# Performance work log

Hardware: AMD Instinct MI355X
Metric: run time of the kernel (lower is better)

Reference implementation:

```python
import jax, jax.numpy as jnp
import numpy as np

N = 100000       # nodes
E = 1600000      # edges (avg degree 16)
IN_DIM = 64
HID_DIM = 128
OUT_DIM = 64

def setup_inputs() -> dict:
    key = jax.random.key(0)
    k = jax.random.split(key, 8)
    inp = jax.random.normal(k[0], (IN_DIM, N), dtype=jnp.float32)
    src = jax.random.randint(k[1], (E,), 0, N, dtype=jnp.int32)
    dst = jax.random.randint(k[2], (E,), 0, N, dtype=jnp.int32)
    # Linear params (torch nn.Linear: y = x @ W.T + b)
    s1 = 1.0 / np.sqrt(IN_DIM)
    W1 = jax.random.uniform(k[3], (HID_DIM, IN_DIM), jnp.float32, -s1, s1)
    b1 = jax.random.uniform(k[4], (HID_DIM,), jnp.float32, -s1, s1)
    s2 = 1.0 / np.sqrt(HID_DIM)
    W2 = jax.random.uniform(k[5], (OUT_DIM, HID_DIM), jnp.float32, -s2, s2)
    b2 = jax.random.uniform(k[6], (OUT_DIM,), jnp.float32, -s2, s2)
    return {"inp": inp, "src": src, "dst": dst, "W1": W1, "b1": b1, "W2": W2, "b2": b2}

def reference(inp, src, dst, W1, b1, W2, b2):
    # inp: [in_dim, N] (module passes transposed features)
    X = inp.T                                   # [N, in_dim] node features
    # update_all(copy_src, sum): gather src features, scatter-add at dst
    agg = jax.ops.segment_sum(X[src], dst, num_segments=X.shape[0])  # [N, in_dim]
    h = jax.nn.relu(agg @ W1.T + b1)            # [N, hidden]
    out = h @ W2.T + b2                         # [N, out_dim]
    return out.T                                 # [out_dim, N] (final .t())
```

## Files before the change

kernel.cpp:

```cpp
#include <hip/hip_runtime.h>
#include <hip/hip_bf16.h>
#include <stdint.h>

typedef unsigned short ushort_t;
using short8   = __attribute__((ext_vector_type(8))) short;
using float4v  = __attribute__((ext_vector_type(4))) float;
using uint4v   = __attribute__((ext_vector_type(4))) unsigned;

#define BSH    6
#define BUCKW  64
#define CAP    1536
#define NBMAX  2048
#define BINB   256

__device__ __forceinline__ float bf2f(ushort_t u) {
    union { unsigned int i; float f; } v;
    v.i = ((unsigned int)u) << 16;
    return v.f;
}
__device__ __forceinline__ ushort_t f2b(float f) {
    union { float f; unsigned int i; } v;
    v.f = f;
    unsigned int u = v.i;
    unsigned int r = (u + 0x7fffu + ((u >> 16) & 1u)) >> 16;
    return (ushort_t)r;
}
__device__ __forceinline__ float blo2f(unsigned v) {
    union { unsigned i; float f; } u; u.i = v << 16; return u.f;
}
__device__ __forceinline__ float bhi2f(unsigned v) {
    union { unsigned i; float f; } u; u.i = v & 0xFFFF0000u; return u.f;
}

__global__ __launch_bounds__(512) void prep_k(
        const float* __restrict__ inp, ushort_t* __restrict__ X, int N,
        const float* __restrict__ W1, const float* __restrict__ W2,
        ushort_t* __restrict__ w1b, ushort_t* __restrict__ w2b,
        const int* __restrict__ src, const int* __restrict__ dst,
        int* __restrict__ gcur, unsigned* __restrict__ bin, int E,
        int NB, int TB) {
    __shared__ int lcnt[NBMAX];
    __shared__ int gbase[NBMAX];
    __shared__ int lcur[NBMAX];
    int tid = threadIdx.x;

    if ((int)blockIdx.x < TB) {
        if (blockIdx.x == 0) {
            for (int i = tid; i < 8192; i += 512) {
                w1b[i] = f2b(W1[i]);
                w2b[i] = f2b(W2[i]);
            }
        }
        int db = tid >> 7;
        int nl = tid & 127;
        int nc = blockIdx.x * 128 + nl;
        if (nc < N) {
            const float* ip = inp + (size_t)(db * 16) * N + nc;
            float v[16];
#pragma unroll
            for (int r = 0; r < 16; ++r)
                v[r] = ip[(size_t)r * N];
            unsigned dw[8];
#pragma unroll
            for (int j = 0; j < 8; ++j)
                dw[j] = (unsigned)f2b(v[2 * j]) | ((unsigned)f2b(v[2 * j + 1]) << 16);
            unsigned* xp = (unsigned*)X + (size_t)nc * 32 + db * 8;
            uint4v a = {dw[0], dw[1], dw[2], dw[3]};
            uint4v b = {dw[4], dw[5], dw[6], dw[7]};
            *(uint4v*)(xp)     = a;
            *(uint4v*)(xp + 4) = b;
        }
    } else {
        int bid   = blockIdx.x - TB;
        int chunk = (E + BINB - 1) / BINB;
        int s0 = bid * chunk;
        int s1 = s0 + chunk;
        if (s1 > E) s1 = E;

        for (int b = tid; b < NB; b += 512) lcnt[b] = 0;
        __syncthreads();

        int e = s0 + tid;
        for (; e + 512 * 7 < s1; e += 512 * 8) {
            int d[8];
#pragma unroll
            for (int k = 0; k < 8; ++k) d[k] = dst[e + 512 * k];
#pragma unroll
            for (int k = 0; k < 8; ++k) atomicAdd(&lcnt[d[k] >> BSH], 1);
        }
        for (; e < s1; e += 512)
            atomicAdd(&lcnt[dst[e] >> BSH], 1);
        __syncthreads();

        for (int b = tid; b < NB; b += 512) {
            int c = lcnt[b];
            gbase[b] = c ? atomicAdd(&gcur[b], c) : 0;
            lcur[b]  = 0;
        }
        __syncthreads();

        e = s0 + tid;
        for (; e + 512 * 7 < s1; e += 512 * 8) {
            int d[8], s[8];
#pragma unroll
            for (int k = 0; k < 8; ++k) {
                d[k] = dst[e + 512 * k];
                s[k] = src[e + 512 * k];
            }
#pragma unroll
            for (int k = 0; k < 8; ++k) {
                int b   = d[k] >> BSH;
                int pos = gbase[b] + atomicAdd(&lcur[b], 1);
                if (pos < CAP)
                    bin[(size_t)b * CAP + pos] =
                        ((unsigned)(d[k] & (BUCKW - 1)) << 24) | (unsigned)s[k];
            }
        }
        for (; e < s1; e += 512) {
            int dv = dst[e];
            int b  = dv >> BSH;
            int pos = gbase[b] + atomicAdd(&lcur[b], 1);
            if (pos < CAP)
                bin[(size_t)b * CAP + pos] =
                    ((unsigned)(dv & (BUCKW - 1)) << 24) | (unsigned)src[e];
        }
    }
}

__global__ __launch_bounds__(256) void bagg_k(
        const unsigned* __restrict__ Xu, const unsigned* __restrict__ bin,
        const int* __restrict__ gcur, unsigned* __restrict__ aggu, int N) {
    __shared__ unsigned sl[CAP];
    __shared__ int ecnt[BUCKW];
    __shared__ int sc[BUCKW];
    __shared__ int ecur[BUCKW];
    int tid = threadIdx.x;
    int b   = blockIdx.x;
    int lo  = b << BSH;

    int cnt = gcur[b];
    if (cnt > CAP) cnt = CAP;
    const unsigned* bb = bin + (size_t)b * CAP;

    if (tid < BUCKW) ecnt[tid] = 0;
    __syncthreads();

    for (int i = tid; i < cnt; i += 256)
        atomicAdd(&ecnt[bb[i] >> 24], 1);
    __syncthreads();

    if (tid < BUCKW) sc[tid] = ecnt[tid];
    __syncthreads();
#pragma unroll
    for (int off = 1; off < BUCKW; off <<= 1) {
        int v = 0;
        if (tid < BUCKW && tid >= off) v = sc[tid - off];
        __syncthreads();
        if (tid < BUCKW) sc[tid] += v;
        __syncthreads();
    }
    if (tid < BUCKW) { sc[tid] -= ecnt[tid]; ecur[tid] = 0; }
    __syncthreads();

    for (int i = tid; i < cnt; i += 256) {
        unsigned p = bb[i];
        int nl  = (int)(p >> 24);
        int pos = sc[nl] + atomicAdd(&ecur[nl], 1);
        sl[pos] = p;
    }
    __syncthreads();

    int wave = tid >> 6;
    int lane = tid & 63;
    int half = lane >> 5;
    int c2   = lane & 31;

    for (int n = wave; n < BUCKW; n += 4) {
        int node = lo + n;
        if (node >= N) break;
        int s0 = sc[n];
        int c  = ecnt[n];
        float alo0 = 0.f, ahi0 = 0.f, alo1 = 0.f, ahi1 = 0.f;
        int i = 0;
        for (; i + 16 <= c; i += 16) {
            unsigned p0 = sl[s0 + i +  0 + half], p1 = sl[s0 + i +  2 + half];
            unsigned p2 = sl[s0 + i +  4 + half], p3 = sl[s0 + i +  6 + half];
            unsigned p4 = sl[s0 + i +  8 + half], p5 = sl[s0 + i + 10 + half];
            unsigned p6 = sl[s0 + i + 12 + half], p7 = sl[s0 + i + 14 + half];
            unsigned v0 = Xu[(size_t)(p0 & 0xFFFFFFu) * 32 + c2];
            unsigned v1 = Xu[(size_t)(p1 & 0xFFFFFFu) * 32 + c2];
            unsigned v2 = Xu[(size_t)(p2 & 0xFFFFFFu) * 32 + c2];
            unsigned v3 = Xu[(size_t)(p3 & 0xFFFFFFu) * 32 + c2];
            unsigned v4 = Xu[(size_t)(p4 & 0xFFFFFFu) * 32 + c2];
            unsigned v5 = Xu[(size_t)(p5 & 0xFFFFFFu) * 32 + c2];
            unsigned v6 = Xu[(size_t)(p6 & 0xFFFFFFu) * 32 + c2];
            unsigned v7 = Xu[(size_t)(p7 & 0xFFFFFFu) * 32 + c2];
            alo0 += blo2f(v0); ahi0 += bhi2f(v0);
            alo1 += blo2f(v1); ahi1 += bhi2f(v1);
            alo0 += blo2f(v2); ahi0 += bhi2f(v2);
            alo1 += blo2f(v3); ahi1 += bhi2f(v3);
            alo0 += blo2f(v4); ahi0 += bhi2f(v4);
            alo1 += blo2f(v5); ahi1 += bhi2f(v5);
            alo0 += blo2f(v6); ahi0 += bhi2f(v6);
            alo1 += blo2f(v7); ahi1 += bhi2f(v7);
        }
        for (; i + 2 <= c; i += 2) {
            unsigned p = sl[s0 + i + half];
            unsigned v = Xu[(size_t)(p & 0xFFFFFFu) * 32 + c2];
            alo0 += blo2f(v); ahi0 += bhi2f(v);
        }
        if (i + half < c) {
            unsigned p = sl[s0 + i + half];
            unsigned v = Xu[(size_t)(p & 0xFFFFFFu) * 32 + c2];
            alo1 += blo2f(v); ahi1 += bhi2f(v);
        }
        float alo = alo0 + alo1;
        float ahi = ahi0 + ahi1;
        float blo = __shfl(alo, lane + 32);
        float bhi = __shfl(ahi, lane + 32);
        if (half == 0) {
            alo += blo; ahi += bhi;
            aggu[(size_t)node * 32 + c2] =
                (unsigned)f2b(alo) | ((unsigned)f2b(ahi) << 16);
        }
    }
}

#define HPITCH 136

__global__ __launch_bounds__(256) void mlp_k(
        const ushort_t* __restrict__ aggb,
        const ushort_t* __restrict__ W1, const float* __restrict__ b1,
        const ushort_t* __restrict__ W2, const float* __restrict__ b2,
        float* __restrict__ out, int N) {
    __shared__ ushort_t h_s[4][16 * HPITCH];

    int wave = threadIdx.x >> 6;
    int lane = threadIdx.x & 63;
    int row  = lane & 15;
    int quad = lane >> 4;
    int n0   = blockIdx.x * 64 + wave * 16;

    int anode = n0 + row;
    if (anode > N - 1) anode = N - 1;
    const ushort_t* ap = aggb + (size_t)anode * 64;
    short8 a0 = *(const short8*)(ap + quad * 8);
    short8 a1 = *(const short8*)(ap + 32 + quad * 8);

    float4v zero = {0.f, 0.f, 0.f, 0.f};
    float4v acc[8];
#pragma unroll
    for (int nt = 0; nt < 8; ++nt) acc[nt] = zero;

#pragma unroll
    for (int nt = 0; nt < 8; ++nt) {
        const ushort_t* wp = W1 + (size_t)(nt * 16 + row) * 64 + quad * 8;
        short8 bf0 = *(const short8*)(wp);
        short8 bf1 = *(const short8*)(wp + 32);
        acc[nt] = __builtin_amdgcn_mfma_f32_16x16x32_bf16(a0, bf0, acc[nt], 0, 0, 0);
        acc[nt] = __builtin_amdgcn_mfma_f32_16x16x32_bf16(a1, bf1, acc[nt], 0, 0, 0);
    }

    ushort_t* hw = h_s[wave];
#pragma unroll
    for (int nt = 0; nt < 8; ++nt) {
        float bias = b1[nt * 16 + row];
#pragma unroll
        for (int r = 0; r < 4; ++r) {
            float v = acc[nt][r] + bias;
            v = v > 0.f ? v : 0.f;
            hw[(quad * 4 + r) * HPITCH + nt * 16 + row] = f2b(v);
        }
    }
    __syncthreads();

    short8 a2[4];
#pragma unroll
    for (int kt = 0; kt < 4; ++kt)
        a2[kt] = *(const short8*)(hw + row * HPITCH + kt * 32 + quad * 8);

    float4v acc2[4];
#pragma unroll
    for (int nt = 0; nt < 4; ++nt) acc2[nt] = zero;

#pragma unroll
    for (int nt = 0; nt < 4; ++nt) {
#pragma unroll
        for (int kt = 0; kt < 4; ++kt) {
            short8 bfr = *(const short8*)(W2 + (size_t)(nt * 16 + row) * 128 +
                                          kt * 32 + quad * 8);
            acc2[nt] = __builtin_amdgcn_mfma_f32_16x16x32_bf16(a2[kt], bfr, acc2[nt], 0, 0, 0);
        }
    }

    int node = n0 + quad * 4;
    if (node < N) {
#pragma unroll
        for (int nt = 0; nt < 4; ++nt) {
            int ko = nt * 16 + row;
            float bias = b2[ko];
            float4v pk;
#pragma unroll
            for (int r = 0; r < 4; ++r) pk[r] = acc2[nt][r] + bias;
            *(float4v*)(out + (size_t)ko * N + node) = pk;
        }
    }
}

extern "C" void kernel_launch(void* const* d_in, const int* in_sizes, int n_in,
                              void* d_out, int out_size, void* d_ws, size_t ws_size,
                              hipStream_t stream) {
    const float* inp = (const float*)d_in[0];
    const int*   src = (const int*)d_in[1];
    const int*   dst = (const int*)d_in[2];
    const float* W1  = (const float*)d_in[3];
    const float* b1  = (const float*)d_in[4];
    const float* W2  = (const float*)d_in[5];
    const float* b2  = (const float*)d_in[6];
    float* out = (float*)d_out;

    int N  = in_sizes[0] / 64;
    int E  = in_sizes[1];
    int NB = (N + BUCKW - 1) >> BSH;

    ushort_t* aggb = (ushort_t*)d_ws;
    ushort_t* w1b  = aggb + (size_t)N * 64;
    ushort_t* w2b  = w1b + 8192;
    int*      gcur = (int*)(w2b + 8192);

    char*     ob  = (char*)d_out;
    ushort_t* X   = (ushort_t*)ob;
    unsigned* bin = (unsigned*)(ob + (size_t)N * 64 * 2);

    hipMemsetAsync(gcur, 0, NB * sizeof(int), stream);

    int TB = (N + 127) / 128;
    prep_k<<<TB + BINB, 512, 0, stream>>>(inp, X, N, W1, W2, w1b, w2b,
                                          src, dst, gcur, bin, E, NB, TB);

    bagg_k<<<NB, 256, 0, stream>>>((const unsigned*)X, bin, gcur,
                                   (unsigned*)aggb, N);

    int tb = (N + 63) / 64;
    mlp_k<<<tb, 256, 0, stream>>>(aggb, w1b, b1, w2b, b2, out, N);
}
```

Measured before the change: 203.2 us.

## Fuse bucket aggregation with MLP in one kernel and widen prep blocks

Adds a fused kernel that aggregates each 64-node bucket into shared memory and runs both MFMA linear layers on it directly. This drops the global round trip of the aggregated bf16 features and one kernel launch. The shared pool is reused for the edge list and the hidden tile. The prep kernel moves to 1024-thread blocks with int4 vectorized edge loads and 32-bit index math. The fused path runs only when the workspace can hold X and the bins; otherwise the old three-kernel path is kept.

Result: slower. 212.7 us (+4.7%).

```diff
diff --git a/kernel.cpp b/kernel.cpp
--- a/kernel.cpp
+++ b/kernel.cpp
@@ -12,6 +12,8 @@
 #define CAP    1536
 #define NBMAX  2048
 #define BINB   256
+#define HPITCH 136
+#define APITCH 36
 
 __device__ __forceinline__ float bf2f(ushort_t u) {
     union { unsigned int i; float f; } v;
@@ -32,97 +34,280 @@
     union { unsigned i; float f; } u; u.i = v & 0xFFFF0000u; return u.f;
 }
 
-__global__ __launch_bounds__(512) void prep_k(
+__global__ __launch_bounds__(1024) void prep_k(
         const float* __restrict__ inp, ushort_t* __restrict__ X, int N,
         const float* __restrict__ W1, const float* __restrict__ W2,
         ushort_t* __restrict__ w1b, ushort_t* __restrict__ w2b,
         const int* __restrict__ src, const int* __restrict__ dst,
         int* __restrict__ gcur, unsigned* __restrict__ bin, int E,
-        int NB, int TB) {
+        int NB) {
     __shared__ int lcnt[NBMAX];
     __shared__ int gbase[NBMAX];
     __shared__ int lcur[NBMAX];
     int tid = threadIdx.x;
 
-    if ((int)blockIdx.x < TB) {
-        if (blockIdx.x == 0) {
-            for (int i = tid; i < 8192; i += 512) {
+    if ((int)blockIdx.x >= BINB) {
+        int tb = blockIdx.x - BINB;
+        if (tb == 0) {
+            for (int i = tid; i < 8192; i += 1024) {
                 w1b[i] = f2b(W1[i]);
                 w2b[i] = f2b(W2[i]);
             }
         }
-        int db = tid >> 7;
-        int nl = tid & 127;
-        int nc = blockIdx.x * 128 + nl;
+        int db = tid >> 8;
+        int nl = tid & 255;
+        int nc = tb * 256 + nl;
         if (nc < N) {
-            const float* ip = inp + (size_t)(db * 16) * N + nc;
+            unsigned ib = (unsigned)(db * 16) * (unsigned)N + (unsigned)nc;
             float v[16];
 #pragma unroll
             for (int r = 0; r < 16; ++r)
-                v[r] = ip[(size_t)r * N];
+                v[r] = inp[ib + (unsigned)(r * N)];
             unsigned dw[8];
 #pragma unroll
             for (int j = 0; j < 8; ++j)
                 dw[j] = (unsigned)f2b(v[2 * j]) | ((unsigned)f2b(v[2 * j + 1]) << 16);
-            unsigned* xp = (unsigned*)X + (size_t)nc * 32 + db * 8;
+            unsigned* xp = (unsigned*)X + (((unsigned)nc) << 5) + (unsigned)(db << 3);
             uint4v a = {dw[0], dw[1], dw[2], dw[3]};
             uint4v b = {dw[4], dw[5], dw[6], dw[7]};
             *(uint4v*)(xp)     = a;
             *(uint4v*)(xp + 4) = b;
         }
     } else {
-        int bid   = blockIdx.x - TB;
-        int chunk = (E + BINB - 1) / BINB;
-        int s0 = bid * chunk;
-        int s1 = s0 + chunk;
-        if (s1 > E) s1 = E;
-
-        for (int b = tid; b < NB; b += 512) lcnt[b] = 0;
-        __syncthreads();
-
-        int e = s0 + tid;
-        for (; e + 512 * 7 < s1; e += 512 * 8) {
-            int d[8];
-#pragma unroll
-            for (int k = 0; k < 8; ++k) d[k] = dst[e + 512 * k];
-#pragma unroll
-            for (int k = 0; k < 8; ++k) atomicAdd(&lcnt[d[k] >> BSH], 1);
-        }
-        for (; e < s1; e += 512)
-            atomicAdd(&lcnt[dst[e] >> BSH], 1);
-        __syncthreads();
-
-        for (int b = tid; b < NB; b += 512) {
+        int bid  = blockIdx.x;
+        int Q    = (E + 3) >> 2;
+        int chunk = (Q + BINB - 1) / BINB;
+        int q0 = bid * chunk;
+        int q1 = q0 + chunk;
+        if (q1 > Q) q1 = Q;
+        const int4* dst4 = (const int4*)dst;
+        const int4* src4 = (const int4*)src;
+
+        for (int b = tid; b < NB; b += 1024) lcnt[b] = 0;
+        __syncthreads();
+
+        for (int q = q0 + tid; q < q1; q += 1024) {
+            int e = q << 2;
+            if (e + 3 < E) {
+                int4 d = dst4[q];
+                atomicAdd(&lcnt[d.x >> BSH], 1);
+                atomicAdd(&lcnt[d.y >> BSH], 1);
+                atomicAdd(&lcnt[d.z >> BSH], 1);
+                atomicAdd(&lcnt[d.w >> BSH], 1);
+            } else {
+                for (int k = e; k < E; ++k) atomicAdd(&lcnt[dst[k] >> BSH], 1);
+            }
+        }
+        __syncthreads();
+
+        for (int b = tid; b < NB; b += 1024) {
             int c = lcnt[b];
             gbase[b] = c ? atomicAdd(&gcur[b], c) : 0;
             lcur[b]  = 0;
         }
         __syncthreads();
 
-        e = s0 + tid;
-        for (; e + 512 * 7 < s1; e += 512 * 8) {
-            int d[8], s[8];
-#pragma unroll
-            for (int k = 0; k < 8; ++k) {
-                d[k] = dst[e + 512 * k];
-                s[k] = src[e + 512 * k];
+        for (int q = q0 + tid; q < q1; q += 1024) {
+            int e = q << 2;
+            if (e + 3 < E) {
+                int4 d = dst4[q];
+                int4 s = src4[q];
+                int dv[4] = {d.x, d.y, d.z, d.w};
+                int sv[4] = {s.x, s.y, s.z, s.w};
+#pragma unroll
+                for (int k = 0; k < 4; ++k) {
+                    int b   = dv[k] >> BSH;
+                    int pos = gbase[b] + atomicAdd(&lcur[b], 1);
+                    if (pos < CAP)
+                        bin[(size_t)b * CAP + pos] =
+                            ((unsigned)(dv[k] & (BUCKW - 1)) << 24) | (unsigned)sv[k];
+                }
+            } else {
+                for (int k = e; k < E; ++k) {
+                    int dv = dst[k];
+                    int b  = dv >> BSH;
+                    int pos = gbase[b] + atomicAdd(&lcur[b], 1);
+                    if (pos < CAP)
+                        bin[(size_t)b * CAP + pos] =
+                            ((unsigned)(dv & (BUCKW - 1)) << 24) | (unsigned)src[k];
+                }
             }
-#pragma unroll
-            for (int k = 0; k < 8; ++k) {
-                int b   = d[k] >> BSH;
-                int pos = gbase[b] + atomicAdd(&lcur[b], 1);
-                if (pos < CAP)
-                    bin[(size_t)b * CAP + pos] =
-                        ((unsigned)(d[k] & (BUCKW - 1)) << 24) | (unsigned)s[k];
+        }
+    }
+}
+
+__global__ __launch_bounds__(256, 5) void bam_k(
+        const unsigned* __restrict__ Xu, const unsigned* __restrict__ bin,
+        const int* __restrict__ gcur,
+        const ushort_t* __restrict__ W1, const float* __restrict__ b1,
+        const ushort_t* __restrict__ W2, const float* __restrict__ b2,
+        float* __restrict__ out, int N) {
+    __shared__ unsigned agg_s[BUCKW * APITCH];
+    __shared__ __align__(16) char pool[4 * 16 * HPITCH * 2];
+    unsigned* sl  = (unsigned*)pool;
+    int* ecnt = (int*)(pool + CAP * 4);
+    int* sc   = ecnt + BUCKW;
+    int* ecur = sc + BUCKW;
+
+    int tid = threadIdx.x;
+    int b   = blockIdx.x;
+
+    int cnt = gcur[b];
+    if (cnt > CAP) cnt = CAP;
+    const unsigned* bb = bin + (size_t)b * CAP;
+
+    if (tid < BUCKW) ecnt[tid] = 0;
+    __syncthreads();
+
+    for (int i = tid; i < cnt; i += 256)
+        atomicAdd(&ecnt[bb[i] >> 24], 1);
+    __syncthreads();
+
+    if (tid < BUCKW) sc[tid] = ecnt[tid];
+    __syncthreads();
+#pragma unroll
+    for (int off = 1; off < BUCKW; off <<= 1) {
+        int v = 0;
+        if (tid < BUCKW && tid >= off) v = sc[tid - off];
+        __syncthreads();
+        if (tid < BUCKW) sc[tid] += v;
+        __syncthreads();
+    }
+    if (tid < BUCKW) { sc[tid] -= ecnt[tid]; ecur[tid] = 0; }
+    __syncthreads();
+
+    for (int i = tid; i < cnt; i += 256) {
+        unsigned p = bb[i];
+        int nl  = (int)(p >> 24);
+        int pos = sc[nl] + atomicAdd(&ecur[nl], 1);
+        sl[pos] = p;
+    }
+    __syncthreads();
+
+    int wave = tid >> 6;
+    int lane = tid & 63;
+    int half = lane >> 5;
+    unsigned cu = (unsigned)(lane & 31);
+
+    for (int n = wave; n < BUCKW; n += 4) {
+        int s0 = sc[n];
+        int c  = ecnt[n];
+        float alo0 = 0.f, ahi0 = 0.f, alo1 = 0.f, ahi1 = 0.f;
+        int i = 0;
+        for (; i + 16 <= c; i += 16) {
+            unsigned p0 = sl[s0 + i +  0 + half], p1 = sl[s0 + i +  2 + half];
+            unsigned p2 = sl[s0 + i +  4 + half], p3 = sl[s0 + i +  6 + half];
+            unsigned p4 = sl[s0 + i +  8 + half], p5 = sl[s0 + i + 10 + half];
+            unsigned p6 = sl[s0 + i + 12 + half], p7 = sl[s0 + i + 14 + half];
+            unsigned v0 = Xu[((p0 & 0xFFFFFFu) << 5) | cu];
+            unsigned v1 = Xu[((p1 & 0xFFFFFFu) << 5) | cu];
+            unsigned v2 = Xu[((p2 & 0xFFFFFFu) << 5) | cu];
+            unsigned v3 = Xu[((p3 & 0xFFFFFFu) << 5) | cu];
+            unsigned v4 = Xu[((p4 & 0xFFFFFFu) << 5) | cu];
+            unsigned v5 = Xu[((p5 & 0xFFFFFFu) << 5) | cu];
+            unsigned v6 = Xu[((p6 & 0xFFFFFFu) << 5) | cu];
+            unsigned v7 = Xu[((p7 & 0xFFFFFFu) << 5) | cu];
+            alo0 += blo2f(v0); ahi0 += bhi2f(v0);
+            alo1 += blo2f(v1); ahi1 += bhi2f(v1);
+            alo0 += blo2f(v2); ahi0 += bhi2f(v2);
+            alo1 += blo2f(v3); ahi1 += bhi2f(v3);
+            alo0 += blo2f(v4); ahi0 += bhi2f(v4);
+            alo1 += blo2f(v5); ahi1 += bhi2f(v5);
+            alo0 += blo2f(v6); ahi0 += bhi2f(v6);
+            alo1 += blo2f(v7); ahi1 += bhi2f(v7);
+        }
+        for (; i + 2 <= c; i += 2) {
+            unsigned p = sl[s0 + i + half];
+            unsigned v = Xu[((p & 0xFFFFFFu) << 5) | cu];
+            alo0 += blo2f(v); ahi0 += bhi2f(v);
+        }
+        if (i + half < c) {
+            unsigned p = sl[s0 + i + half];
+            unsigned v = Xu[((p & 0xFFFFFFu) << 5) | cu];
+            alo1 += blo2f(v); ahi1 += bhi2f(v);
+        }
+        float alo = alo0 + alo1;
+        float ahi = ahi0 + ahi1;
+        float blo = __shfl(alo, lane + 32);
+        float bhi = __shfl(ahi, lane + 32);
+        if (half == 0) {
+            alo += blo; ahi += bhi;
+            agg_s[n * APITCH + (int)cu] =
+                (unsigned)f2b(alo) | ((unsigned)f2b(ahi) << 16);
+        }
+    }
+    __syncthreads();
+
+    ushort_t* hw = (ushort_t*)pool + (size_t)wave * (16 * HPITCH);
+    int row  = lane & 15;
+    int quad = lane >> 4;
+
+    const unsigned* arow = agg_s + (wave * 16 + row) * APITCH;
+    short8 a0 = *(const short8*)(arow + quad * 4);
+    short8 a1 = *(const short8*)(arow + 16 + quad * 4);
+
+    float4v zero = {0.f, 0.f, 0.f, 0.f};
+
+#pragma unroll
+    for (int g = 0; g < 2; ++g) {
+        float4v acc[4];
+#pragma unroll
+        for (int nt = 0; nt < 4; ++nt) acc[nt] = zero;
+#pragma unroll
+        for (int nt = 0; nt < 4; ++nt) {
+            const ushort_t* wp = W1 + (size_t)(g * 64 + nt * 16 + row) * 64 + quad * 8;
+            short8 bf0 = *(const short8*)(wp);
+            short8 bf1 = *(const short8*)(wp + 32);
+            acc[nt] = __builtin_amdgcn_mfma_f32_16x16x32_bf16(a0, bf0, acc[nt], 0, 0, 0);
+            acc[nt] = __builtin_amdgcn_mfma_f32_16x16x32_bf16(a1, bf1, acc[nt], 0, 0, 0);
+        }
+#pragma unroll
+        for (int nt = 0; nt < 4; ++nt) {
+            float bias = b1[g * 64 + nt * 16 + row];
+#pragma unroll
+            for (int r = 0; r < 4; ++r) {
+                float v = acc[nt][r] + bias;
+                v = v > 0.f ? v : 0.f;
+                hw[(quad * 4 + r) * HPITCH + g * 64 + nt * 16 + row] = f2b(v);
             }
         }
-        for (; e < s1; e += 512) {
-            int dv = dst[e];
-            int b  = dv >> BSH;
-            int pos = gbase[b] + atomicAdd(&lcur[b], 1);
-            if (pos < CAP)
-                bin[(size_t)b * CAP + pos] =
-                    ((unsigned)(dv & (BUCKW - 1)) << 24) | (unsigned)src[e];
+    }
+    __syncthreads();
+
+    short8 a2[4];
+#pragma unroll
+    for (int kt = 0; kt < 4; ++kt)
+        a2[kt] = *(const short8*)(hw + row * HPITCH + kt * 32 + quad * 8);
+
+    float4v acc2[4];
+#pragma unroll
+    for (int nt = 0; nt < 4; ++nt) acc2[nt] = zero;
+
+#pragma unroll
+    for (int nt = 0; nt < 4; ++nt) {
+#pragma unroll
+        for (int kt = 0; kt < 4; ++kt) {
+            short8 bfr = *(const short8*)(W2 + (size_t)(nt * 16 + row) * 128 +
+                                          kt * 32 + quad * 8);
+            acc2[nt] = __builtin_amdgcn_mfma_f32_16x16x32_bf16(a2[kt], bfr, acc2[nt], 0, 0, 0);
+        }
+    }
+
+    int n0   = (b << BSH) + wave * 16;
+    int node = n0 + quad * 4;
+#pragma unroll
+    for (int nt = 0; nt < 4; ++nt) {
+        int ko = nt * 16 + row;
+        float bias = b2[ko];
+        float4v pk;
+#pragma unroll
+        for (int r = 0; r < 4; ++r) pk[r] = acc2[nt][r] + bias;
+        if (node + 3 < N) {
+            *(float4v*)(out + (size_t)ko * N + node) = pk;
+        } else {
+#pragma unroll
+            for (int r = 0; r < 4; ++r)
+                if (node + r < N) out[(size_t)ko * N + node + r] = pk[r];
         }
     }
 }
@@ -144,11 +329,9 @@
 
     if (tid < BUCKW) ecnt[tid] = 0;
     __syncthreads();
-
     for (int i = tid; i < cnt; i += 256)
         atomicAdd(&ecnt[bb[i] >> 24], 1);
     __syncthreads();
-
     if (tid < BUCKW) sc[tid] = ecnt[tid];
     __syncthreads();
 #pragma unroll
@@ -161,7 +344,6 @@
     }
     if (tid < BUCKW) { sc[tid] -= ecnt[tid]; ecur[tid] = 0; }
     __syncthreads();
-
     for (int i = tid; i < cnt; i += 256) {
         unsigned p = bb[i];
         int nl  = (int)(p >> 24);
@@ -173,7 +355,7 @@
     int wave = tid >> 6;
     int lane = tid & 63;
     int half = lane >> 5;
-    int c2   = lane & 31;
+    unsigned cu = (unsigned)(lane & 31);
 
     for (int n = wave; n < BUCKW; n += 4) {
         int node = lo + n;
@@ -187,14 +369,14 @@
             unsigned p2 = sl[s0 + i +  4 + half], p3 = sl[s0 + i +  6 + half];
             unsigned p4 = sl[s0 + i +  8 + half], p5 = sl[s0 + i + 10 + half];
             unsigned p6 = sl[s0 + i + 12 + half], p7 = sl[s0 + i + 14 + half];
-            unsigned v0 = Xu[(size_t)(p0 & 0xFFFFFFu) * 32 + c2];
-            unsigned v1 = Xu[(size_t)(p1 & 0xFFFFFFu) * 32 + c2];
-            unsigned v2 = Xu[(size_t)(p2 & 0xFFFFFFu) * 32 + c2];
-            unsigned v3 = Xu[(size_t)(p3 & 0xFFFFFFu) * 32 + c2];
-            unsigned v4 = Xu[(size_t)(p4 & 0xFFFFFFu) * 32 + c2];
-            unsigned v5 = Xu[(size_t)(p5 & 0xFFFFFFu) * 32 + c2];
-            unsigned v6 = Xu[(size_t)(p6 & 0xFFFFFFu) * 32 + c2];
-            unsigned v7 = Xu[(size_t)(p7 & 0xFFFFFFu) * 32 + c2];
+            unsigned v0 = Xu[((p0 & 0xFFFFFFu) << 5) | cu];
+            unsigned v1 = Xu[((p1 & 0xFFFFFFu) << 5) | cu];
+            unsigned v2 = Xu[((p2 & 0xFFFFFFu) << 5) | cu];
+            unsigned v3 = Xu[((p3 & 0xFFFFFFu) << 5) | cu];
+            unsigned v4 = Xu[((p4 & 0xFFFFFFu) << 5) | cu];
+            unsigned v5 = Xu[((p5 & 0xFFFFFFu) << 5) | cu];
+            unsigned v6 = Xu[((p6 & 0xFFFFFFu) << 5) | cu];
+            unsigned v7 = Xu[((p7 & 0xFFFFFFu) << 5) | cu];
             alo0 += blo2f(v0); ahi0 += bhi2f(v0);
             alo1 += blo2f(v1); ahi1 += bhi2f(v1);
             alo0 += blo2f(v2); ahi0 += bhi2f(v2);
@@ -206,12 +388,12 @@
         }
         for (; i + 2 <= c; i += 2) {
             unsigned p = sl[s0 + i + half];
-            unsigned v = Xu[(size_t)(p & 0xFFFFFFu) * 32 + c2];
+            unsigned v = Xu[((p & 0xFFFFFFu) << 5) | cu];
             alo0 += blo2f(v); ahi0 += bhi2f(v);
         }
         if (i + half < c) {
             unsigned p = sl[s0 + i + half];
-            unsigned v = Xu[(size_t)(p & 0xFFFFFFu) * 32 + c2];
+            unsigned v = Xu[((p & 0xFFFFFFu) << 5) | cu];
             alo1 += blo2f(v); ahi1 += bhi2f(v);
         }
         float alo = alo0 + alo1;
@@ -220,13 +402,11 @@
         float bhi = __shfl(ahi, lane + 32);
         if (half == 0) {
             alo += blo; ahi += bhi;
-            aggu[(size_t)node * 32 + c2] =
+            aggu[(size_t)node * 32 + (int)cu] =
                 (unsigned)f2b(alo) | ((unsigned)f2b(ahi) << 16);
         }
     }
 }
-
-#define HPITCH 136
 
 __global__ __launch_bounds__(256) void mlp_k(
         const ushort_t* __restrict__ aggb,
@@ -323,24 +503,46 @@
     int E  = in_sizes[1];
     int NB = (N + BUCKW - 1) >> BSH;
 
-    ushort_t* aggb = (ushort_t*)d_ws;
-    ushort_t* w1b  = aggb + (size_t)N * 64;
-    ushort_t* w2b  = w1b + 8192;
-    int*      gcur = (int*)(w2b + 8192);
-
-    char*     ob  = (char*)d_out;
-    ushort_t* X   = (ushort_t*)ob;
-    unsigned* bin = (unsigned*)(ob + (size_t)N * 64 * 2);
-
-    hipMemsetAsync(gcur, 0, NB * sizeof(int), stream);
-
-    int TB = (N + 127) / 128;
-    prep_k<<<TB + BINB, 512, 0, stream>>>(inp, X, N, W1, W2, w1b, w2b,
-                                          src, dst, gcur, bin, E, NB, TB);
-
-    bagg_k<<<NB, 256, 0, stream>>>((const unsigned*)X, bin, gcur,
-                                   (unsigned*)aggb, N);
-
-    int tb = (N + 63) / 64;
-    mlp_k<<<tb, 256, 0, stream>>>(aggb, w1b, b1, w2b, b2, out, N);
-}
+    size_t xBytes   = (size_t)N * 64 * 2;
+    size_t binBytes = (size_t)NB * CAP * 4;
+    size_t fusedNeed = xBytes + binBytes + 2 * 8192 * 2 + NBMAX * 4 + 256;
+
+    int TB = (N + 255) / 256;
+
+    if (ws_size >= fusedNeed) {
+        char* w = (char*)d_ws;
+        ushort_t* X    = (ushort_t*)w;
+        unsigned* bin  = (unsigned*)(w + xBytes);
+        ushort_t* w1b  = (ushort_t*)(w + xBytes + binBytes);
+        ushort_t* w2b  = w1b + 8192;
+        int*      gcur = (int*)(w2b + 8192);
+
+        hipMemsetAsync(gcur, 0, NB * sizeof(int), stream);
+
+        prep_k<<<BINB + TB, 1024, 0, stream>>>(inp, X, N, W1, W2, w1b, w2b,
+                                               src, dst, gcur, bin, E, NB);
+
+        bam_k<<<NB, 256, 0, stream>>>((const unsigned*)X, bin, gcur,
+                                      w1b, b1, w2b, b2, out, N);
+    } else {
+        ushort_t* aggb = (ushort_t*)d_ws;
+        ushort_t* w1b  = aggb + (size_t)N * 64;
+        ushort_t* w2b  = w1b + 8192;
+        int*      gcur = (int*)(w2b + 8192);
+
+        char*     ob  = (char*)d_out;
+        ushort_t* X   = (ushort_t*)ob;
+        unsigned* bin = (unsigned*)(ob + xBytes);
+
+        hipMemsetAsync(gcur, 0, NB * sizeof(int), stream);
+
+        prep_k<<<BINB + TB, 1024, 0, stream>>>(inp, X, N, W1, W2, w1b, w2b,
+                                               src, dst, gcur, bin, E, NB);
+
+        bagg_k<<<NB, 256, 0, stream>>>((const unsigned*)X, bin, gcur,
+                                       (unsigned*)aggb, N);
+
+        int tb = (N + 63) / 64;
+        mlp_k<<<tb, 256, 0, stream>>>(aggb, w1b, b1, w2b, b2, out, N);
+    }
+}
```
